# Kernel tuning notes

Hardware: AMD Instinct MI355X
Metric: run time of the kernel (lower is better)

Reference implementation:

```python
import jax, jax.numpy as jnp
import numpy as np

EPS = 1e-6

def masked_softmax(x, m, axis):
    # Faithful to KrantikariQA tensor_utils.masked_softmax:
    #   x = x*m; e = exp(x - max(x)) * m; e / (sum(e) + 1e-6)
    x = x * m
    ex = jnp.exp(x - jnp.max(x, axis=axis, keepdims=True)) * m
    return ex / (jnp.sum(ex, axis=axis, keepdims=True) + EPS)

def setup_inputs() -> dict:
    key = jax.random.key(0)
    k = jax.random.split(key, 7)
    Lq, Lp, B, D = 256, 256, 64, 1024
    q = jax.random.normal(k[0], (Lq, B, D), jnp.float32)
    p = jax.random.normal(k[1], (Lp, B, D), jnp.float32)
    qm = jax.random.randint(k[2], (B, Lq), 0, 2).astype(jnp.int32)
    pm = jax.random.randint(k[3], (B, Lp), 0, 2).astype(jnp.int32)
    # nn.Linear weights (out, in), no bias
    WF = jax.random.normal(k[4], (D, D), jnp.float32) * 0.02
    WG = jax.random.normal(k[5], (D, 2 * D), jnp.float32) * 0.02
    WH = jax.random.normal(k[6], (1, 2 * D), jnp.float32) * 0.02
    return {"q": q, "p": p, "qm": qm, "pm": pm, "WF": WF, "WG": WG, "WH": WH}

def reference(q, p, qm, pm, WF, WG, WH):
    # Attend: att = F(x), batch-first [B, L, D]
    att_q = jnp.einsum('lbd,ed->ble', q, WF)          # [B,Lq,D]
    att_p = jnp.einsum('lbd,ed->ble', p, WF)          # [B,Lp,D]
    e = jnp.einsum('bqe,bpe->bqp', att_q, att_p)      # [B,Lq,Lp]
    m = qm.astype(q.dtype)[:, :, None] * pm.astype(q.dtype)[:, None, :]  # [B,Lq,Lp]
    softmax_j = masked_softmax(e, m, axis=2)                              # over Lp
    softmax_i = masked_softmax(e.transpose(0, 2, 1), m.transpose(0, 2, 1), axis=2)  # [B,Lp,Lq]
    beta = jnp.einsum('bqp,pbd->bqd', softmax_j, p)   # [B,Lq,D]
    alpha = jnp.einsum('bpq,qbd->bpd', softmax_i, q)  # [B,Lp,D]
    # Compare
    v1 = jnp.concatenate([q.transpose(1, 0, 2), beta], axis=-1) @ WG.T   # [B,Lq,D]
    v2 = jnp.concatenate([p.transpose(1, 0, 2), alpha], axis=-1) @ WG.T  # [B,Lp,D]
    # Aggregate
    sum_v1 = jnp.sum(v1, axis=1)  # [B,D]
    sum_v2 = jnp.sum(v2, axis=1)  # [B,D]
    return jnp.concatenate([sum_v1, sum_v2], axis=-1) @ WH.T  # [B,1]
```

## Files before the change

### kernel.cpp

```cpp
#include <hip/hip_runtime.h>

typedef _Float16 f16x8 __attribute__((ext_vector_type(8)));
using f32x4 = __attribute__((ext_vector_type(4))) float;

constexpr int B = 64, L = 256, D = 1024;
constexpr int BD = B * D;
constexpr float EPS = 1e-6f;

__device__ __forceinline__ void gload_lds16(const void* g, void* l) {
    __builtin_amdgcn_global_load_lds((const __attribute__((address_space(1))) void*)g,
                                     (__attribute__((address_space(3))) void*)l,
                                     16, 0, 0);
}

__global__ __launch_bounds__(256) void k_cvt4(const float* __restrict__ q,
                                              const float* __restrict__ p,
                                              short* __restrict__ q16,
                                              short* __restrict__ p16) {
    const int t = blockIdx.x * 256 + threadIdx.x;
    const int j0 = t, j1 = t + 1048576;
    const float4* q4 = (const float4*)q;
    const float4* p4 = (const float4*)p;
    float4 a0 = q4[2 * j0], a1 = q4[2 * j0 + 1];
    float4 b0 = q4[2 * j1], b1 = q4[2 * j1 + 1];
    float4 c0 = p4[2 * j0], c1 = p4[2 * j0 + 1];
    float4 d0 = p4[2 * j1], d1 = p4[2 * j1 + 1];
    union { _Float16 h[8]; int4 v; } ua, ub, uc, ud;
    ua.h[0]=(_Float16)a0.x; ua.h[1]=(_Float16)a0.y; ua.h[2]=(_Float16)a0.z; ua.h[3]=(_Float16)a0.w;
    ua.h[4]=(_Float16)a1.x; ua.h[5]=(_Float16)a1.y; ua.h[6]=(_Float16)a1.z; ua.h[7]=(_Float16)a1.w;
    ub.h[0]=(_Float16)b0.x; ub.h[1]=(_Float16)b0.y; ub.h[2]=(_Float16)b0.z; ub.h[3]=(_Float16)b0.w;
    ub.h[4]=(_Float16)b1.x; ub.h[5]=(_Float16)b1.y; ub.h[6]=(_Float16)b1.z; ub.h[7]=(_Float16)b1.w;
    uc.h[0]=(_Float16)c0.x; uc.h[1]=(_Float16)c0.y; uc.h[2]=(_Float16)c0.z; uc.h[3]=(_Float16)c0.w;
    uc.h[4]=(_Float16)c1.x; uc.h[5]=(_Float16)c1.y; uc.h[6]=(_Float16)c1.z; uc.h[7]=(_Float16)c1.w;
    ud.h[0]=(_Float16)d0.x; ud.h[1]=(_Float16)d0.y; ud.h[2]=(_Float16)d0.z; ud.h[3]=(_Float16)d0.w;
    ud.h[4]=(_Float16)d1.x; ud.h[5]=(_Float16)d1.y; ud.h[6]=(_Float16)d1.z; ud.h[7]=(_Float16)d1.w;
    ((int4*)q16)[j0] = ua.v;
    ((int4*)q16)[j1] = ub.v;
    ((int4*)p16)[j0] = uc.v;
    ((int4*)p16)[j1] = ud.v;
}

__global__ __launch_bounds__(256) void k_wfgp(const float* __restrict__ WF,
                                              const float* __restrict__ WG,
                                              const float* __restrict__ WH,
                                              short* __restrict__ WFt16,
                                              float* __restrict__ gp1,
                                              float* __restrict__ gp2) {
    __shared__ float tile[32][33];
    const int bid = blockIdx.x;
    if (bid < 1024) {
        const int rt = bid >> 5, ct = bid & 31;
        const int t = threadIdx.x;
        const int r = t >> 3, c4 = (t & 7) * 4;
        float4 v = *(const float4*)(WF + (long)(rt * 32 + r) * D + ct * 32 + c4);
        tile[r][c4] = v.x; tile[r][c4 + 1] = v.y; tile[r][c4 + 2] = v.z; tile[r][c4 + 3] = v.w;
        __syncthreads();
        union { _Float16 h[4]; short4 s; } u;
        u.h[0] = (_Float16)tile[c4 + 0][r];
        u.h[1] = (_Float16)tile[c4 + 1][r];
        u.h[2] = (_Float16)tile[c4 + 2][r];
        u.h[3] = (_Float16)tile[c4 + 3][r];
        *(short4*)(WFt16 + (long)(ct * 32 + r) * D + rt * 32 + c4) = u.s;
    } else {
        const int lb = bid - 1024;
        const int kx = lb & 7, ec = lb >> 3;
        const int k = kx * 256 + threadIdx.x;
        const int e0 = ec * 128;
        float a = 0.f, c = 0.f;
        for (int e = 0; e < 128; ++e) {
            float w = WG[(long)(e0 + e) * (2 * D) + k];
            a += w * WH[e0 + e];
            c += w * WH[D + e0 + e];
        }
        gp1[ec * 2048 + k] = a; gp2[ec * 2048 + k] = c;
    }
}

template <int WM, int WN, int MR>
__global__ __launch_bounds__(WM * WN * 64) void k_gemm(
    const short* __restrict__ A, long sA, long bA,
    const short* __restrict__ Bm, long sB, long bB,
    int K, int bx, int per_batch, int f16_out,
    short* __restrict__ Ch, float* __restrict__ Cf, int ldC, long batchC)
{
    constexpr int BM = WM * MR * 16, BN = WN * 64;
    constexpr int T = WM * WN * 64;
    constexpr int TILEB = (BM + BN) * 64;
    constexpr int ROUNDS = TILEB / (T * 16);
    __shared__ __align__(16) char lds[2 * TILEB];

    const int t = threadIdx.x, lane = t & 63, w = t >> 6;
    const int wm = w / WN, wn = w % WN;

    const int lin = blockIdx.x;
    const int chunk = gridDim.x >> 3;
    const int swz = (lin & 7) * chunk + (lin >> 3);
    const int z = swz / per_batch;
    const int r0 = swz % per_batch;
    const int mb = (r0 / bx) * BM, nb = (r0 % bx) * BN;

    const char* Ab = (const char*)A + bA * z;
    const char* Bb = (const char*)Bm + bB * z;

    const char* sp[ROUNDS];
    #pragma unroll
    for (int r = 0; r < ROUNDS; ++r) {
        int g = r * T + t;
        int row = g >> 2, sg = g & 3;
        int lg = sg ^ ((row >> 1) & 3);
        if (row < BM) sp[r] = Ab + (long)(mb + row) * sA + lg * 16;
        else          sp[r] = Bb + (long)(nb + row - BM) * sB + lg * 16;
    }

    int aoff[MR], boff[4];
    #pragma unroll
    for (int i = 0; i < MR; ++i) {
        int ra = wm * (MR * 16) + i * 16 + (lane & 15);
        aoff[i] = ra * 64 + (((lane >> 4) ^ ((ra >> 1) & 3))) * 16;
    }
    #pragma unroll
    for (int j = 0; j < 4; ++j) {
        int rb = wn * 64 + j * 16 + (lane & 15);
        boff[j] = BM * 64 + rb * 64 + (((lane >> 4) ^ ((rb >> 1) & 3))) * 16;
    }

    f32x4 acc[MR][4] = {};
    const int NT = K >> 5;

    {
        #pragma unroll
        for (int r = 0; r < ROUNDS; ++r)
            gload_lds16(sp[r], lds + (r * T + t) * 16);
    }

    int cur = 0;
    for (int kt = 0; kt < NT; ++kt) {
        asm volatile("s_waitcnt vmcnt(0)" ::: "memory");
        __builtin_amdgcn_sched_barrier(0);
        __builtin_amdgcn_s_barrier();
        __builtin_amdgcn_sched_barrier(0);
        if (kt + 1 < NT) {
            long kb = (long)(kt + 1) * 64;
            char* dstb = lds + (cur ^ 1) * TILEB;
            #pragma unroll
            for (int r = 0; r < ROUNDS; ++r)
                gload_lds16(sp[r] + kb, dstb + (r * T + t) * 16);
        }
        __builtin_amdgcn_sched_barrier(0);
        const char* lb = lds + cur * TILEB;
        f16x8 fb[4], fa[MR];
        #pragma unroll
        for (int j = 0; j < 4; ++j) fb[j] = *(const f16x8*)(lb + boff[j]);
        #pragma unroll
        for (int i = 0; i < MR; ++i) fa[i] = *(const f16x8*)(lb + aoff[i]);
        #pragma unroll
        for (int i = 0; i < MR; ++i)
            #pragma unroll
            for (int j = 0; j < 4; ++j)
                acc[i][j] = __builtin_amdgcn_mfma_f32_16x16x32_f16(fb[j], fa[i], acc[i][j], 0, 0, 0);
        cur ^= 1;
    }

    const long zC = batchC * z;
    #pragma unroll
    for (int i = 0; i < MR; ++i)
        #pragma unroll
        for (int j = 0; j < 4; ++j) {
            int row = mb + wm * (MR * 16) + i * 16 + (lane & 15);
            int col = nb + wn * 64 + j * 16 + (lane >> 4) * 4;
            long idx = zC + (long)row * ldC + col;
            if (f16_out) {
                union { _Float16 h[4]; short4 s; } u;
                #pragma unroll
                for (int rr = 0; rr < 4; ++rr) u.h[rr] = (_Float16)acc[i][j][rr];
                *(short4*)(Ch + idx) = u.s;
            } else {
                float4 v = make_float4(acc[i][j][0], acc[i][j][1], acc[i][j][2], acc[i][j][3]);
                *(float4*)(Cf + idx) = v;
            }
        }
}

__global__ __launch_bounds__(256) void k_fold_g(const float* __restrict__ Gp,
                                                short* __restrict__ G16) {
    const int i = blockIdx.x * 256 + threadIdx.x;
    constexpr int N4 = (1 << 20) / 4;
    const float4* g = (const float4*)Gp;
    float4 v0 = g[i], v1 = g[N4 + i], v2 = g[2 * N4 + i], v3 = g[3 * N4 + i];
    union { _Float16 h[4]; short4 s; } u;
    u.h[0] = (_Float16)(v0.x + v1.x + v2.x + v3.x);
    u.h[1] = (_Float16)(v0.y + v1.y + v2.y + v3.y);
    u.h[2] = (_Float16)(v0.z + v1.z + v2.z + v3.z);
    u.h[3] = (_Float16)(v0.w + v1.w + v2.w + v3.w);
    ((short4*)G16)[i] = u.s;
}

__global__ __launch_bounds__(256) void k_pass1(const float* __restrict__ E,
                                               const int* __restrict__ qm,
                                               const int* __restrict__ pm,
                                               float* __restrict__ impart,
                                               float* __restrict__ ispart,
                                               float* __restrict__ cjpart) {
    const int qc = blockIdx.x, b = blockIdx.y;
    const int p = threadIdx.x, lane = p & 63, w = p >> 6;
    const int q0 = qc * 32;
    __shared__ float wred[32][4];
    __shared__ float rowmx[32], rowsm[32], qmv_s[32];
    if (p < 32) qmv_s[p] = (float)qm[b * L + q0 + p];
    __syncthreads();
    const float pmv = (float)pm[b * L + p];
    const float* eb = E + b * (L * L) + q0 * L + p;

    float xv[32];
    float im = -1e30f;
    #pragma unroll
    for (int r = 0; r < 32; ++r) {
        float mm = pmv * qmv_s[r];
        float x = eb[r * L] * mm;
        xv[r] = x;
        im = fmaxf(im, x);
        float v = x;
        #pragma unroll
        for (int o = 32; o; o >>= 1) v = fmaxf(v, __shfl_xor(v, o));
        if (lane == 0) wred[r][w] = v;
    }
    __syncthreads();
    if (p < 32) rowmx[p] = fmaxf(fmaxf(wred[p][0], wred[p][1]), fmaxf(wred[p][2], wred[p][3]));
    __syncthreads();
    float is = 0.f;
    #pragma unroll
    for (int r = 0; r < 32; ++r) {
        float mm = pmv * qmv_s[r];
        is += mm * __expf(xv[r] - im);
        float v = mm * __expf(xv[r] - rowmx[r]);
        #pragma unroll
        for (int o = 32; o; o >>= 1) v += __shfl_xor(v, o);
        if (lane == 0) wred[r][w] = v;
    }
    __syncthreads();
    if (p < 32) rowsm[p] = wred[p][0] + wred[p][1] + wred[p][2] + wred[p][3];
    __syncthreads();
    float cj = 0.f;
    #pragma unroll
    for (int r = 0; r < 32; ++r) {
        float mm = pmv * qmv_s[r];
        cj += mm * __expf(xv[r] - rowmx[r]) / (rowsm[r] + EPS);
    }
    const int o = (b * 8 + qc) * 256 + p;
    impart[o] = im; ispart[o] = is; cjpart[o] = cj;
}

__global__ __launch_bounds__(256) void k_combine(const float* __restrict__ impart,
                                                 const float* __restrict__ ispart,
                                                 const float* __restrict__ cjpart,
                                                 float* __restrict__ rmi,
                                                 float* __restrict__ rsi,
                                                 float* __restrict__ colj) {
    const int b = blockIdx.x, p = threadIdx.x;
    const int base = b * 8 * 256 + p;
    float m = -1e30f, s = 0.f, c = 0.f;
    #pragma unroll
    for (int k = 0; k < 8; ++k) m = fmaxf(m, impart[base + k * 256]);
    #pragma unroll
    for (int k = 0; k < 8; ++k) {
        s += ispart[base + k * 256] * __expf(impart[base + k * 256] - m);
        c += cjpart[base + k * 256];
    }
    rmi[b * L + p] = m; rsi[b * L + p] = s; colj[b * L + p] = c;
}

__global__ __launch_bounds__(256) void k_colsum_i(const float* __restrict__ E,
                                                  const int* __restrict__ qm,
                                                  const int* __restrict__ pm,
                                                  const float* __restrict__ rmaxi,
                                                  const float* __restrict__ rsumi,
                                                  float* __restrict__ coli) {
    const int wid = threadIdx.x >> 6, lane = threadIdx.x & 63;
    const int row = blockIdx.x * 4 + wid;
    const int b = row >> 8;
    const float qmv = (float)qm[row];
    const float* er = E + row * L;
    float acc = 0.f;
    #pragma unroll
    for (int i = 0; i < 4; ++i) {
        int pp = lane + 64 * i;
        float mm = qmv * (float)pm[b * L + pp];
        float x = er[pp] * mm;
        acc += mm * __expf(x - rmaxi[b * L + pp]) / (rsumi[b * L + pp] + EPS);
    }
    #pragma unroll
    for (int o = 32; o; o >>= 1) acc += __shfl_xor(acc, o);
    if (lane == 0) coli[row] = acc;
}

__global__ __launch_bounds__(128) void k_sums2(const short* __restrict__ Q16,
                                               const short* __restrict__ P16,
                                               const float* __restrict__ colj,
                                               const float* __restrict__ coli,
                                               float* __restrict__ pq,
                                               float* __restrict__ pp,
                                               float* __restrict__ pb,
                                               float* __restrict__ pa) {
    const int c = blockIdx.x, b = blockIdx.y, t = threadIdx.x;
    const int d0 = t * 8;
    float aq[8] = {}, ap[8] = {}, ab[8] = {}, aa[8] = {};
    for (int l = c * 64; l < c * 64 + 64; ++l) {
        union { int4 v; _Float16 h[8]; } uq, up;
        uq.v = *(const int4*)(Q16 + (long)l * BD + b * D + d0);
        up.v = *(const int4*)(P16 + (long)l * BD + b * D + d0);
        float cj = colj[b * L + l], ci = coli[b * L + l];
        #pragma unroll
        for (int k = 0; k < 8; ++k) {
            float qf = (float)uq.h[k], pf = (float)up.h[k];
            aq[k] += qf; ap[k] += pf; ab[k] += cj * pf; aa[k] += ci * qf;
        }
    }
    const long o = ((long)c * B + b) * D + d0;
    *(float4*)(pq + o) = make_float4(aq[0], aq[1], aq[2], aq[3]);
    *(float4*)(pq + o + 4) = make_float4(aq[4], aq[5], aq[6], aq[7]);
    *(float4*)(pp + o) = make_float4(ap[0], ap[1], ap[2], ap[3]);
    *(float4*)(pp + o + 4) = make_float4(ap[4], ap[5], ap[6], ap[7]);
    *(float4*)(pb + o) = make_float4(ab[0], ab[1], ab[2], ab[3]);
    *(float4*)(pb + o + 4) = make_float4(ab[4], ab[5], ab[6], ab[7]);
    *(float4*)(pa + o) = make_float4(aa[0], aa[1], aa[2], aa[3]);
    *(float4*)(pa + o + 4) = make_float4(aa[4], aa[5], aa[6], aa[7]);
}

__global__ __launch_bounds__(256) void k_final2(const float* __restrict__ pq,
                                                const float* __restrict__ pp,
                                                const float* __restrict__ pb,
                                                const float* __restrict__ pa,
                                                const float* __restrict__ gp1,
                                                const float* __restrict__ gp2,
                                                float* __restrict__ out) {
    const int b = blockIdx.x, t = threadIdx.x;
    float acc = 0.f;
    for (int d = t; d < D; d += 256) {
        float sq = 0.f, sp_ = 0.f, sb = 0.f, sa = 0.f;
        #pragma unroll
        for (int c2 = 0; c2 < 4; ++c2) {
            long o = ((long)c2 * B + b) * D + d;
            sq += pq[o]; sp_ += pp[o]; sb += pb[o]; sa += pa[o];
        }
        float g1d = 0.f, g1D = 0.f, g2d = 0.f, g2D = 0.f;
        #pragma unroll
        for (int ec = 0; ec < 8; ++ec) {
            g1d += gp1[ec * 2048 + d];     g1D += gp1[ec * 2048 + D + d];
            g2d += gp2[ec * 2048 + d];     g2D += gp2[ec * 2048 + D + d];
        }
        acc += sq * g1d + sb * g1D + sp_ * g2d + sa * g2D;
    }
    #pragma unroll
    for (int o = 32; o; o >>= 1) acc += __shfl_xor(acc, o);
    __shared__ float red[4];
    const int wid = t >> 6, lane = t & 63;
    if (lane == 0) red[wid] = acc;
    __syncthreads();
    if (t == 0) out[b] = red[0] + red[1] + red[2] + red[3];
}

extern "C" void kernel_launch(void* const* d_in, const int* in_sizes, int n_in,
                              void* d_out, int out_size, void* d_ws, size_t ws_size,
                              hipStream_t stream) {
    const float* q  = (const float*)d_in[0];
    const float* p  = (const float*)d_in[1];
    const int*   qm = (const int*)d_in[2];
    const int*   pm = (const int*)d_in[3];
    const float* WF = (const float*)d_in[4];
    const float* WG = (const float*)d_in[5];
    const float* WH = (const float*)d_in[6];
    float* out = (float*)d_out;

    char* wsb = (char*)d_ws;
    short* q16   = (short*)(wsb);
    short* p16   = (short*)(wsb + (32l << 20));
    short* T16   = (short*)(wsb + (64l << 20));
    short* WFt16 = (short*)(wsb + (96l << 20));
    short* G16   = (short*)(wsb + (98l << 20));
    float* Gp    = (float*)(wsb + (100l << 20));
    float* E     = (float*)(wsb + (100l << 20));
    float* st    = (float*)(wsb + (116l << 20));
    const int BL = B * L;
    float* impart = st;                  float* ispart = impart + B * 8 * 256;
    float* cjpart = ispart + B * 8 * 256;
    float* rmi  = cjpart + B * 8 * 256;  float* rsi  = rmi + BL;
    float* colj = rsi + BL;              float* coli = colj + BL;
    float* pq   = coli + BL;             float* pp   = pq + 4 * BD;
    float* pb   = pp + 4 * BD;           float* pa   = pb + 4 * BD;
    float* gp1  = pa + 4 * BD;           float* gp2  = gp1 + 8 * 2048;

    k_cvt4<<<4096, 256, 0, stream>>>(q, p, q16, p16);
    k_wfgp<<<1088, 256, 0, stream>>>(WF, WG, WH, WFt16, gp1, gp2);
    k_gemm<2, 2, 4><<<256, 256, 0, stream>>>(WFt16, 2048, 512, WFt16, 2048, 512,
                                             256, 8, 64, 0, nullptr, Gp, 1024, 1l << 20);
    k_fold_g<<<1024, 256, 0, stream>>>(Gp, G16);
    k_gemm<2, 4, 8><<<256, 512, 0, stream>>>(q16, 2048, 0, G16, 2048, 0,
                                             1024, 4, 256, 1, T16, nullptr, 1024, 0);
    k_gemm<2, 2, 4><<<256, 256, 0, stream>>>(T16, 64l * 2048, 2048, p16, 64l * 2048, 2048,
                                             1024, 2, 4, 0, nullptr, E, 256, 65536);
    k_pass1<<<dim3(8, B), 256, 0, stream>>>(E, qm, pm, impart, ispart, cjpart);
    k_combine<<<B, 256, 0, stream>>>(impart, ispart, cjpart, rmi, rsi, colj);
    k_colsum_i<<<BL / 4, 256, 0, stream>>>(E, qm, pm, rmi, rsi, coli);
    k_sums2<<<dim3(4, B), 128, 0, stream>>>(q16, p16, colj, coli, pq, pp, pb, pa);
    k_final2<<<B, 256, 0, stream>>>(pq, pp, pb, pa, gp1, gp2, out);
}
```

Before: 182.9 us.

## Fuse fp32-to-fp16 conversion of q and p into GEMM tile loads

Drops the standalone conversion kernel and instead has the GEMMs read fp32 q/p directly. They convert to fp16 in registers and store to LDS after the MFMA work, while the other operand still uses direct global-to-LDS loads. The reduction kernel now reads fp32 q/p too. This removes one launch and the write and re-read of the fp16 copies, in exchange for twice the global read bytes per GEMM tile and register-staged loads that may pipeline less well.

```diff
diff --git a/kernel.cpp b/kernel.cpp
--- a/kernel.cpp
+++ b/kernel.cpp
@@ -11,33 +11,6 @@
     __builtin_amdgcn_global_load_lds((const __attribute__((address_space(1))) void*)g,
                                      (__attribute__((address_space(3))) void*)l,
                                      16, 0, 0);
-}
-
-__global__ __launch_bounds__(256) void k_cvt4(const float* __restrict__ q,
-                                              const float* __restrict__ p,
-                                              short* __restrict__ q16,
-                                              short* __restrict__ p16) {
-    const int t = blockIdx.x * 256 + threadIdx.x;
-    const int j0 = t, j1 = t + 1048576;
-    const float4* q4 = (const float4*)q;
-    const float4* p4 = (const float4*)p;
-    float4 a0 = q4[2 * j0], a1 = q4[2 * j0 + 1];
-    float4 b0 = q4[2 * j1], b1 = q4[2 * j1 + 1];
-    float4 c0 = p4[2 * j0], c1 = p4[2 * j0 + 1];
-    float4 d0 = p4[2 * j1], d1 = p4[2 * j1 + 1];
-    union { _Float16 h[8]; int4 v; } ua, ub, uc, ud;
-    ua.h[0]=(_Float16)a0.x; ua.h[1]=(_Float16)a0.y; ua.h[2]=(_Float16)a0.z; ua.h[3]=(_Float16)a0.w;
-    ua.h[4]=(_Float16)a1.x; ua.h[5]=(_Float16)a1.y; ua.h[6]=(_Float16)a1.z; ua.h[7]=(_Float16)a1.w;
-    ub.h[0]=(_Float16)b0.x; ub.h[1]=(_Float16)b0.y; ub.h[2]=(_Float16)b0.z; ub.h[3]=(_Float16)b0.w;
-    ub.h[4]=(_Float16)b1.x; ub.h[5]=(_Float16)b1.y; ub.h[6]=(_Float16)b1.z; ub.h[7]=(_Float16)b1.w;
-    uc.h[0]=(_Float16)c0.x; uc.h[1]=(_Float16)c0.y; uc.h[2]=(_Float16)c0.z; uc.h[3]=(_Float16)c0.w;
-    uc.h[4]=(_Float16)c1.x; uc.h[5]=(_Float16)c1.y; uc.h[6]=(_Float16)c1.z; uc.h[7]=(_Float16)c1.w;
-    ud.h[0]=(_Float16)d0.x; ud.h[1]=(_Float16)d0.y; ud.h[2]=(_Float16)d0.z; ud.h[3]=(_Float16)d0.w;
-    ud.h[4]=(_Float16)d1.x; ud.h[5]=(_Float16)d1.y; ud.h[6]=(_Float16)d1.z; ud.h[7]=(_Float16)d1.w;
-    ((int4*)q16)[j0] = ua.v;
-    ((int4*)q16)[j1] = ub.v;
-    ((int4*)p16)[j0] = uc.v;
-    ((int4*)p16)[j1] = ud.v;
 }
 
 __global__ __launch_bounds__(256) void k_wfgp(const float* __restrict__ WF,
@@ -76,10 +49,10 @@
     }
 }
 
-template <int WM, int WN, int MR>
+template <int WM, int WN, int MR, int A32, int B32>
 __global__ __launch_bounds__(WM * WN * 64) void k_gemm(
-    const short* __restrict__ A, long sA, long bA,
-    const short* __restrict__ Bm, long sB, long bB,
+    const char* __restrict__ A, long sA, long bA,
+    const char* __restrict__ Bm, long sB, long bB,
     int K, int bx, int per_batch, int f16_out,
     short* __restrict__ Ch, float* __restrict__ Cf, int ldC, long batchC)
 {
@@ -87,6 +60,7 @@
     constexpr int T = WM * WN * 64;
     constexpr int TILEB = (BM + BN) * 64;
     constexpr int ROUNDS = TILEB / (T * 16);
+    constexpr int ROUNDS_A = (BM * 4) / T;
     __shared__ __align__(16) char lds[2 * TILEB];
 
     const int t = threadIdx.x, lane = t & 63, w = t >> 6;
@@ -99,8 +73,8 @@
     const int r0 = swz % per_batch;
     const int mb = (r0 / bx) * BM, nb = (r0 % bx) * BN;
 
-    const char* Ab = (const char*)A + bA * z;
-    const char* Bb = (const char*)Bm + bB * z;
+    const char* Ab = A + bA * z;
+    const char* Bb = Bm + bB * z;
 
     const char* sp[ROUNDS];
     #pragma unroll
@@ -108,8 +82,8 @@
         int g = r * T + t;
         int row = g >> 2, sg = g & 3;
         int lg = sg ^ ((row >> 1) & 3);
-        if (row < BM) sp[r] = Ab + (long)(mb + row) * sA + lg * 16;
-        else          sp[r] = Bb + (long)(nb + row - BM) * sB + lg * 16;
+        if (r < ROUNDS_A) sp[r] = Ab + (long)(mb + row) * sA + lg * (A32 ? 32 : 16);
+        else              sp[r] = Bb + (long)(nb + row - BM) * sB + lg * (B32 ? 32 : 16);
     }
 
     int aoff[MR], boff[4];
@@ -129,8 +103,20 @@
 
     {
         #pragma unroll
-        for (int r = 0; r < ROUNDS; ++r)
-            gload_lds16(sp[r], lds + (r * T + t) * 16);
+        for (int r = 0; r < ROUNDS; ++r) {
+            const bool is32 = (r < ROUNDS_A) ? (A32 != 0) : (B32 != 0);
+            if (is32) {
+                float4 s0 = *(const float4*)(sp[r]);
+                float4 s1 = *(const float4*)(sp[r] + 16);
+                union { _Float16 h[8]; int4 v; } u;
+                u.h[0]=(_Float16)s0.x; u.h[1]=(_Float16)s0.y; u.h[2]=(_Float16)s0.z; u.h[3]=(_Float16)s0.w;
+                u.h[4]=(_Float16)s1.x; u.h[5]=(_Float16)s1.y; u.h[6]=(_Float16)s1.z; u.h[7]=(_Float16)s1.w;
+                *((int4*)(lds + (r * T + t) * 16)) = u.v;
+            } else {
+                gload_lds16(sp[r], lds + (r * T + t) * 16);
+            }
+        }
+        asm volatile("s_waitcnt lgkmcnt(0)" ::: "memory");
     }
 
     int cur = 0;
@@ -139,12 +125,20 @@
         __builtin_amdgcn_sched_barrier(0);
         __builtin_amdgcn_s_barrier();
         __builtin_amdgcn_sched_barrier(0);
+        float4 stg[ROUNDS][2];
+        char* dstb = lds + (cur ^ 1) * TILEB;
         if (kt + 1 < NT) {
-            long kb = (long)(kt + 1) * 64;
-            char* dstb = lds + (cur ^ 1) * TILEB;
             #pragma unroll
-            for (int r = 0; r < ROUNDS; ++r)
-                gload_lds16(sp[r] + kb, dstb + (r * T + t) * 16);
+            for (int r = 0; r < ROUNDS; ++r) {
+                const bool is32 = (r < ROUNDS_A) ? (A32 != 0) : (B32 != 0);
+                long kb = (long)(kt + 1) * (is32 ? 128 : 64);
+                if (is32) {
+                    stg[r][0] = *(const float4*)(sp[r] + kb);
+                    stg[r][1] = *(const float4*)(sp[r] + kb + 16);
+                } else {
+                    gload_lds16(sp[r] + kb, dstb + (r * T + t) * 16);
+                }
+            }
         }
         __builtin_amdgcn_sched_barrier(0);
         const char* lb = lds + cur * TILEB;
@@ -158,6 +152,22 @@
             #pragma unroll
             for (int j = 0; j < 4; ++j)
                 acc[i][j] = __builtin_amdgcn_mfma_f32_16x16x32_f16(fb[j], fa[i], acc[i][j], 0, 0, 0);
+        if ((A32 || B32) && (kt + 1 < NT)) {
+            #pragma unroll
+            for (int r = 0; r < ROUNDS; ++r) {
+                const bool is32 = (r < ROUNDS_A) ? (A32 != 0) : (B32 != 0);
+                if (is32) {
+                    union { _Float16 h[8]; int4 v; } u;
+                    u.h[0]=(_Float16)stg[r][0].x; u.h[1]=(_Float16)stg[r][0].y;
+                    u.h[2]=(_Float16)stg[r][0].z; u.h[3]=(_Float16)stg[r][0].w;
+                    u.h[4]=(_Float16)stg[r][1].x; u.h[5]=(_Float16)stg[r][1].y;
+                    u.h[6]=(_Float16)stg[r][1].z; u.h[7]=(_Float16)stg[r][1].w;
+                    *((int4*)(dstb + (r * T + t) * 16)) = u.v;
+                }
+            }
+            asm volatile("s_waitcnt lgkmcnt(0)" ::: "memory");
+            __builtin_amdgcn_sched_barrier(0);
+        }
         cur ^= 1;
     }
 
@@ -293,8 +303,8 @@
     if (lane == 0) coli[row] = acc;
 }
 
-__global__ __launch_bounds__(128) void k_sums2(const short* __restrict__ Q16,
-                                               const short* __restrict__ P16,
+__global__ __launch_bounds__(128) void k_sums2(const float* __restrict__ Q,
+                                               const float* __restrict__ P,
                                                const float* __restrict__ colj,
                                                const float* __restrict__ coli,
                                                float* __restrict__ pq,
@@ -305,14 +315,16 @@
     const int d0 = t * 8;
     float aq[8] = {}, ap[8] = {}, ab[8] = {}, aa[8] = {};
     for (int l = c * 64; l < c * 64 + 64; ++l) {
-        union { int4 v; _Float16 h[8]; } uq, up;
-        uq.v = *(const int4*)(Q16 + (long)l * BD + b * D + d0);
-        up.v = *(const int4*)(P16 + (long)l * BD + b * D + d0);
+        const float* qp = Q + (long)l * BD + b * D + d0;
+        const float* pp_ = P + (long)l * BD + b * D + d0;
+        float4 q0 = *(const float4*)qp, q1 = *(const float4*)(qp + 4);
+        float4 p0 = *(const float4*)pp_, p1 = *(const float4*)(pp_ + 4);
         float cj = colj[b * L + l], ci = coli[b * L + l];
+        float qv[8] = {q0.x, q0.y, q0.z, q0.w, q1.x, q1.y, q1.z, q1.w};
+        float pv[8] = {p0.x, p0.y, p0.z, p0.w, p1.x, p1.y, p1.z, p1.w};
         #pragma unroll
         for (int k = 0; k < 8; ++k) {
-            float qf = (float)uq.h[k], pf = (float)up.h[k];
-            aq[k] += qf; ap[k] += pf; ab[k] += cj * pf; aa[k] += ci * qf;
+            aq[k] += qv[k]; ap[k] += pv[k]; ab[k] += cj * pv[k]; aa[k] += ci * qv[k];
         }
     }
     const long o = ((long)c * B + b) * D + d0;
@@ -372,14 +384,12 @@
     float* out = (float*)d_out;
 
     char* wsb = (char*)d_ws;
-    short* q16   = (short*)(wsb);
-    short* p16   = (short*)(wsb + (32l << 20));
-    short* T16   = (short*)(wsb + (64l << 20));
-    short* WFt16 = (short*)(wsb + (96l << 20));
-    short* G16   = (short*)(wsb + (98l << 20));
-    float* Gp    = (float*)(wsb + (100l << 20));
-    float* E     = (float*)(wsb + (100l << 20));
-    float* st    = (float*)(wsb + (116l << 20));
+    short* T16   = (short*)(wsb);
+    short* WFt16 = (short*)(wsb + (32l << 20));
+    short* G16   = (short*)(wsb + (34l << 20));
+    float* Gp    = (float*)(wsb + (36l << 20));
+    float* E     = (float*)(wsb + (36l << 20));
+    float* st    = (float*)(wsb + (52l << 20));
     const int BL = B * L;
     float* impart = st;                  float* ispart = impart + B * 8 * 256;
     float* cjpart = ispart + B * 8 * 256;
@@ -389,18 +399,20 @@
     float* pb   = pp + 4 * BD;           float* pa   = pb + 4 * BD;
     float* gp1  = pa + 4 * BD;           float* gp2  = gp1 + 8 * 2048;
 
-    k_cvt4<<<4096, 256, 0, stream>>>(q, p, q16, p16);
     k_wfgp<<<1088, 256, 0, stream>>>(WF, WG, WH, WFt16, gp1, gp2);
-    k_gemm<2, 2, 4><<<256, 256, 0, stream>>>(WFt16, 2048, 512, WFt16, 2048, 512,
-                                             256, 8, 64, 0, nullptr, Gp, 1024, 1l << 20);
+    k_gemm<2, 2, 4, 0, 0><<<256, 256, 0, stream>>>(
+        (const char*)WFt16, 2048, 512, (const char*)WFt16, 2048, 512,
+        256, 8, 64, 0, nullptr, Gp, 1024, 1l << 20);
     k_fold_g<<<1024, 256, 0, stream>>>(Gp, G16);
-    k_gemm<2, 4, 8><<<256, 512, 0, stream>>>(q16, 2048, 0, G16, 2048, 0,
-                                             1024, 4, 256, 1, T16, nullptr, 1024, 0);
-    k_gemm<2, 2, 4><<<256, 256, 0, stream>>>(T16, 64l * 2048, 2048, p16, 64l * 2048, 2048,
-                                             1024, 2, 4, 0, nullptr, E, 256, 65536);
+    k_gemm<2, 4, 8, 1, 0><<<256, 512, 0, stream>>>(
+        (const char*)q, 4096, 0, (const char*)G16, 2048, 0,
+        1024, 4, 256, 1, T16, nullptr, 1024, 0);
+    k_gemm<2, 2, 4, 0, 1><<<256, 256, 0, stream>>>(
+        (const char*)T16, 64l * 2048, 2048, (const char*)p, 64l * 4096, 4096,
+        1024, 2, 4, 0, nullptr, E, 256, 65536);
     k_pass1<<<dim3(8, B), 256, 0, stream>>>(E, qm, pm, impart, ispart, cjpart);
     k_combine<<<B, 256, 0, stream>>>(impart, ispart, cjpart, rmi, rsi, colj);
     k_colsum_i<<<BL / 4, 256, 0, stream>>>(E, qm, pm, rmi, rsi, coli);
-    k_sums2<<<dim3(4, B), 128, 0, stream>>>(q16, p16, colj, coli, pq, pp, pb, pa);
+    k_sums2<<<dim3(4, B), 128, 0, stream>>>(q, p, colj, coli, pq, pp, pb, pa);
     k_final2<<<B, 256, 0, stream>>>(pq, pp, pb, pa, gp1, gp2, out);
 }
```

Measured after the change: 165.3 us. 9.6% less time.
